# Kernel tuning notes

Measured on AMD Instinct MI355X. Metric: run time of the kernel, lower is better.

Reference implementation:

```python
import jax, jax.numpy as jnp
import numpy as np

N = 512
D = 400          # per-sample feature dim (lstm_hidden_dim * 2)
H = 400          # hidden dim of F_func (lstm_hidden_dim * 2)


def setup_inputs() -> dict:
    key = jax.random.key(0)
    k1, k2, k3, k4, k5, k6 = jax.random.split(key, 6)
    x_samples = jax.random.normal(k1, (N, D), dtype=jnp.float32)
    y_samples = jax.random.normal(k2, (N, D), dtype=jnp.float32)
    # torch nn.Linear default init: U(-1/sqrt(fan_in), 1/sqrt(fan_in))
    b1_bound = 1.0 / np.sqrt(2 * D)
    b2_bound = 1.0 / np.sqrt(H)
    W1 = jax.random.uniform(k3, (H, 2 * D), minval=-b1_bound, maxval=b1_bound, dtype=jnp.float32)
    b1 = jax.random.uniform(k4, (H,), minval=-b1_bound, maxval=b1_bound, dtype=jnp.float32)
    W2 = jax.random.uniform(k5, (1, H), minval=-b2_bound, maxval=b2_bound, dtype=jnp.float32)
    b2 = jax.random.uniform(k6, (1,), minval=-b2_bound, maxval=b2_bound, dtype=jnp.float32)
    return {"x_samples": x_samples, "y_samples": y_samples,
            "W1": W1, "b1": b1, "W2": W2, "b2": b2}


def reference(x_samples, y_samples, W1, b1, W2, b2):
    n = y_samples.shape[0]
    W1x, W1y = W1[:, :D], W1[:, D:]
    hx = x_samples @ W1x.T          # [N, H], contribution of x
    hy = y_samples @ W1y.T          # [N, H], contribution of y

    def score(h):  # second linear + softplus, squeeze out last dim of 1
        return jax.nn.softplus(h @ W2.T + b2)[..., 0]

    # T0[i] = F(x[i], y[i])
    T0 = score(jax.nn.relu(hx + hy + b1))                      # [N]
    # T1[i, j] = F(x[j], y[i])  (x tiled along dim 0, y along dim 1)
    h_pair = jax.nn.relu(hy[:, None, :] + hx[None, :, :] + b1) # [N, N, H]
    T1 = score(h_pair)                                          # [N, N]

    t0_mean = T0.mean()
    lower_bound = t0_mean - (jax.nn.logsumexp(T1, axis=1).mean() - jnp.log(jnp.float32(n)))
    upper_bound = t0_mean - T1.mean()
    return (lower_bound, upper_bound)
```

## Files before the change

kernel.cpp:

```cpp
#include <hip/hip_runtime.h>
#include <math.h>


#define NSAMP 512
#define DIM 400
#define HID 400

__global__ __launch_bounds__(256) void club_gemm_kernel(
    const float* __restrict__ X, const float* __restrict__ Y,
    const float* __restrict__ W1, const float* __restrict__ b1,
    float* __restrict__ hxT8, float* __restrict__ hyb)
{
    __shared__ __align__(16) float Ls[64 * 204];
    const int t    = threadIdx.x;
    const int lane = t & 63;
    const int wave = __builtin_amdgcn_readfirstlane(t >> 6);
    const int b    = blockIdx.x;

    const float* __restrict__ Lbase;
    const float* __restrict__ Sbase;
    int Lstride, Lcol0, Lrow0, Lrowmax, Sstride, srow_base;
    int kh, mat;

    if (b < 400) {
        mat = 0; kh = b & 1;
        const int bx = (b >> 1) & 7, by = b >> 4;
        Lbase = X;  Lstride = DIM;     Lcol0 = 0;   Lrow0 = bx * 64; Lrowmax = NSAMP - 1;
        Sbase = W1; Sstride = 2 * DIM;
        srow_base = by * 16 + wave * 4;
    } else {
        mat = 1;
        const int bb = b - 400; kh = bb & 1;
        const int bx = (bb >> 1) & 31, by = bb >> 6;
        Lbase = W1; Lstride = 2 * DIM; Lcol0 = DIM; Lrow0 = by * 64; Lrowmax = HID - 1;
        Sbase = Y;  Sstride = DIM;
        srow_base = bx * 16 + wave * 4;
    }
    const int kc0 = kh * 200;

    for (int idx = t; idx < 3200; idx += 256) {
        int row = idx / 50, q = idx % 50;
        int r = Lrow0 + row; if (r > Lrowmax) r = Lrowmax;
        float4 v = *(const float4*)(Lbase + (size_t)r * Lstride + Lcol0 + kc0 + 4 * q);
        *(float4*)(Ls + row * 204 + 4 * q) = v;
    }
    __syncthreads();

    float acc[4] = {0.f, 0.f, 0.f, 0.f};
#pragma unroll 2
    for (int k4 = 0; k4 < 50; k4++) {
        float4 xv = *(const float4*)(Ls + lane * 204 + 4 * k4);
#pragma unroll
        for (int c = 0; c < 4; c++) {
            const float* __restrict__ wp =
                Sbase + (size_t)(srow_base + c) * Sstride + Lcol0 - (mat ? DIM : 0)
                      + (mat ? 0 : 0) + kc0 + 4 * k4;
            float4 wv = *(const float4*)(Sbase + (size_t)(srow_base + c) * Sstride + kc0 + 4 * k4);
            (void)wp;
            acc[c] = fmaf(xv.x, wv.x, acc[c]);
            acc[c] = fmaf(xv.y, wv.y, acc[c]);
            acc[c] = fmaf(xv.z, wv.z, acc[c]);
            acc[c] = fmaf(xv.w, wv.w, acc[c]);
        }
    }

    if (mat == 0) {
        const int j = Lrow0 + lane;
        float* __restrict__ base =
            hxT8 + (size_t)(srow_base >> 3) * 4096 + (size_t)j * 8 + (srow_base & 4);
#pragma unroll
        for (int c = 0; c < 4; c++)
            atomicAdd(base + c, acc[c]);
    } else {
        const int h = Lrow0 + lane;
        if (h < HID) {
            if (kh == 0) {
                float bv = b1[h];
#pragma unroll
                for (int c = 0; c < 4; c++) acc[c] += bv;
            }
#pragma unroll
            for (int c = 0; c < 4; c++)
                atomicAdd(hyb + (size_t)(srow_base + c) * HID + h, acc[c]);
        }
    }
}

__global__ __launch_bounds__(256) void club_pair_kernel(
    const float* __restrict__ hxT8, const float* __restrict__ hyb,
    const float* __restrict__ W2, const float* __restrict__ b2,
    double* __restrict__ expsum, double* __restrict__ tsum,
    double* __restrict__ diagT)
{
    const int t    = threadIdx.x;
    const int lane = t & 63;
    const int wave = __builtin_amdgcn_readfirstlane(t >> 6);
    const int jx   = blockIdx.x;
    const int j    = jx * 64 + lane;
    const int i    = blockIdx.y * 4 + wave;

    const float* __restrict__ Bp = hxT8 + (size_t)j * 8;
    const float* __restrict__ Ap = hyb + (size_t)i * HID;

    float acc0 = 0.f, acc1 = 0.f;
#pragma unroll 2
    for (int g = 0; g < 50; g++) {
        const int h = 8 * g;
        float4 b0 = *(const float4*)(Bp + (size_t)g * 4096);
        float4 b1v = *(const float4*)(Bp + (size_t)g * 4096 + 4);
        float4 a0 = *(const float4*)(Ap + h);
        float4 a1 = *(const float4*)(Ap + h + 4);
        float4 w0 = *(const float4*)(W2 + h);
        float4 w1 = *(const float4*)(W2 + h + 4);
        acc0 = fmaf(fmaxf(a0.x + b0.x, 0.f), w0.x, acc0);
        acc1 = fmaf(fmaxf(a0.y + b0.y, 0.f), w0.y, acc1);
        acc0 = fmaf(fmaxf(a0.z + b0.z, 0.f), w0.z, acc0);
        acc1 = fmaf(fmaxf(a0.w + b0.w, 0.f), w0.w, acc1);
        acc0 = fmaf(fmaxf(a1.x + b1v.x, 0.f), w1.x, acc0);
        acc1 = fmaf(fmaxf(a1.y + b1v.y, 0.f), w1.y, acc1);
        acc0 = fmaf(fmaxf(a1.z + b1v.z, 0.f), w1.z, acc0);
        acc1 = fmaf(fmaxf(a1.w + b1v.w, 0.f), w1.w, acc1);
    }

    float s  = (acc0 + acc1) + b2[0];
    float es = expf(s);
    float T  = log1pf(es);
    if (j == i) diagT[i] = (double)T;
    double eD = 1.0 + (double)es;
    double tD = (double)T;
    for (int off = 32; off > 0; off >>= 1) {
        eD += __shfl_down(eD, off);
        tD += __shfl_down(tD, off);
    }
    if (lane == 0) {
        expsum[i * 8 + jx] = eD;
        tsum  [i * 8 + jx] = tD;
    }
}

__global__ __launch_bounds__(512) void club_final_kernel(
    const double* __restrict__ expsum, const double* __restrict__ tsum,
    const double* __restrict__ diagT, float* __restrict__ out)
{
    __shared__ double sh[3 * 512];
    const int t = threadIdx.x;
    double es = 0.0, ts = 0.0;
#pragma unroll
    for (int b = 0; b < 8; b++) { es += expsum[t * 8 + b]; ts += tsum[t * 8 + b]; }
    sh[t] = log(es); sh[512 + t] = ts; sh[1024 + t] = diagT[t];
    __syncthreads();
    for (int off = 256; off > 0; off >>= 1) {
        if (t < off) {
            sh[t]        += sh[t + off];
            sh[512 + t]  += sh[512 + t + off];
            sh[1024 + t] += sh[1024 + t + off];
        }
        __syncthreads();
    }
    if (t == 0) {
        double t0m  = sh[1024] / 512.0;
        double lsem = sh[0]    / 512.0;
        double t1m  = sh[512]  / (512.0 * 512.0);
        out[0] = (float)(t0m - (lsem - log(512.0)));
        out[1] = (float)(t0m - t1m);
    }
}

extern "C" void kernel_launch(void* const* d_in, const int* in_sizes, int n_in,
                              void* d_out, int out_size, void* d_ws, size_t ws_size,
                              hipStream_t stream) {
    const float* X  = (const float*)d_in[0];
    const float* Y  = (const float*)d_in[1];
    const float* W1 = (const float*)d_in[2];
    const float* b1 = (const float*)d_in[3];
    const float* W2 = (const float*)d_in[4];
    const float* b2 = (const float*)d_in[5];
    float* out = (float*)d_out;

    char* ws = (char*)d_ws;
    float*  hxT8   = (float*) (ws);
    float*  hyb    = (float*) (ws +  819200);
    double* expsum = (double*)(ws + 1638400);
    double* tsum   = (double*)(ws + 1671168);
    double* diagT  = (double*)(ws + 1703936);

    hipMemsetAsync(ws, 0, 1638400, stream);

    club_gemm_kernel <<<dim3(848),    256, 0, stream>>>(X, Y, W1, b1, hxT8, hyb);
    club_pair_kernel <<<dim3(8, 128), 256, 0, stream>>>(hxT8, hyb, W2, b2,
                                                        expsum, tsum, diagT);
    club_final_kernel<<<1, 512, 0, stream>>>(expsum, tsum, diagT, out);
}
```

Measured before the change: 112.2 us.

## Drop memset and atomics, fuse final reduction into pair kernel via last-block counter

The GEMM kernel now loops over both K halves itself and writes results directly instead of splitting K and accumulating with atomicAdd. This removes the workspace memset. The pair kernel computes four rows of i per wave group and splits H across two waves, combining the halves through shared memory so each hx load is reused across rows. The separate final kernel is replaced by a last-block-done counter that runs the reduction inside the pair kernel. Together these cut launches and atomics. In exchange the GEMM reads more operand data per block, and the counter reset depends on the GEMM kernel running first.

```diff
diff --git a/kernel.cpp b/kernel.cpp
--- a/kernel.cpp
+++ b/kernel.cpp
@@ -9,79 +9,76 @@
 __global__ __launch_bounds__(256) void club_gemm_kernel(
     const float* __restrict__ X, const float* __restrict__ Y,
     const float* __restrict__ W1, const float* __restrict__ b1,
-    float* __restrict__ hxT8, float* __restrict__ hyb)
+    float* __restrict__ hxT8, float* __restrict__ hyb,
+    unsigned int* __restrict__ counter)
 {
     __shared__ __align__(16) float Ls[64 * 204];
     const int t    = threadIdx.x;
     const int lane = t & 63;
     const int wave = __builtin_amdgcn_readfirstlane(t >> 6);
     const int b    = blockIdx.x;
+    if (b == 0 && t == 0) *counter = 0u;
 
     const float* __restrict__ Lbase;
     const float* __restrict__ Sbase;
-    int Lstride, Lcol0, Lrow0, Lrowmax, Sstride, srow_base;
-    int kh, mat;
+    int Lstride, Lcol0, Lrow0, Lrowmax, Sstride, sr0;
+    int mat;
 
     if (b < 400) {
-        mat = 0; kh = b & 1;
-        const int bx = (b >> 1) & 7, by = b >> 4;
+        mat = 0;
+        const int bx = b & 7, by = b >> 3;
         Lbase = X;  Lstride = DIM;     Lcol0 = 0;   Lrow0 = bx * 64; Lrowmax = NSAMP - 1;
         Sbase = W1; Sstride = 2 * DIM;
-        srow_base = by * 16 + wave * 4;
+        sr0 = by * 8 + wave * 2;
     } else {
         mat = 1;
-        const int bb = b - 400; kh = bb & 1;
-        const int bx = (bb >> 1) & 31, by = bb >> 6;
+        const int bb = b - 400;
+        const int bx = bb & 63, by = bb >> 6;
         Lbase = W1; Lstride = 2 * DIM; Lcol0 = DIM; Lrow0 = by * 64; Lrowmax = HID - 1;
         Sbase = Y;  Sstride = DIM;
-        srow_base = bx * 16 + wave * 4;
-    }
-    const int kc0 = kh * 200;
-
-    for (int idx = t; idx < 3200; idx += 256) {
-        int row = idx / 50, q = idx % 50;
-        int r = Lrow0 + row; if (r > Lrowmax) r = Lrowmax;
-        float4 v = *(const float4*)(Lbase + (size_t)r * Lstride + Lcol0 + kc0 + 4 * q);
-        *(float4*)(Ls + row * 204 + 4 * q) = v;
-    }
-    __syncthreads();
-
-    float acc[4] = {0.f, 0.f, 0.f, 0.f};
+        sr0 = bx * 8 + wave * 2;
+    }
+
+    float acc0 = 0.f, acc1 = 0.f;
+
+    for (int kc = 0; kc < DIM; kc += 200) {
+        __syncthreads();
+        for (int idx = t; idx < 3200; idx += 256) {
+            int row = idx / 50, q = idx % 50;
+            int r = Lrow0 + row; if (r > Lrowmax) r = Lrowmax;
+            float4 v = *(const float4*)(Lbase + (size_t)r * Lstride + Lcol0 + kc + 4 * q);
+            *(float4*)(Ls + row * 204 + 4 * q) = v;
+        }
+        __syncthreads();
+        const float* __restrict__ w0p = Sbase + (size_t)sr0 * Sstride + kc;
+        const float* __restrict__ w1p = Sbase + (size_t)(sr0 + 1) * Sstride + kc;
 #pragma unroll 2
-    for (int k4 = 0; k4 < 50; k4++) {
-        float4 xv = *(const float4*)(Ls + lane * 204 + 4 * k4);
-#pragma unroll
-        for (int c = 0; c < 4; c++) {
-            const float* __restrict__ wp =
-                Sbase + (size_t)(srow_base + c) * Sstride + Lcol0 - (mat ? DIM : 0)
-                      + (mat ? 0 : 0) + kc0 + 4 * k4;
-            float4 wv = *(const float4*)(Sbase + (size_t)(srow_base + c) * Sstride + kc0 + 4 * k4);
-            (void)wp;
-            acc[c] = fmaf(xv.x, wv.x, acc[c]);
-            acc[c] = fmaf(xv.y, wv.y, acc[c]);
-            acc[c] = fmaf(xv.z, wv.z, acc[c]);
-            acc[c] = fmaf(xv.w, wv.w, acc[c]);
+        for (int k4 = 0; k4 < 50; k4++) {
+            float4 xv = *(const float4*)(Ls + lane * 204 + 4 * k4);
+            float4 wa = *(const float4*)(w0p + 4 * k4);
+            float4 wb = *(const float4*)(w1p + 4 * k4);
+            acc0 = fmaf(xv.x, wa.x, acc0);
+            acc0 = fmaf(xv.y, wa.y, acc0);
+            acc0 = fmaf(xv.z, wa.z, acc0);
+            acc0 = fmaf(xv.w, wa.w, acc0);
+            acc1 = fmaf(xv.x, wb.x, acc1);
+            acc1 = fmaf(xv.y, wb.y, acc1);
+            acc1 = fmaf(xv.z, wb.z, acc1);
+            acc1 = fmaf(xv.w, wb.w, acc1);
         }
     }
 
     if (mat == 0) {
+        const int g = sr0 >> 3;
         const int j = Lrow0 + lane;
-        float* __restrict__ base =
-            hxT8 + (size_t)(srow_base >> 3) * 4096 + (size_t)j * 8 + (srow_base & 4);
-#pragma unroll
-        for (int c = 0; c < 4; c++)
-            atomicAdd(base + c, acc[c]);
+        *(float2*)(hxT8 + ((size_t)g * NSAMP + j) * 8 + (sr0 & 7)) =
+            make_float2(acc0, acc1);
     } else {
         const int h = Lrow0 + lane;
         if (h < HID) {
-            if (kh == 0) {
-                float bv = b1[h];
-#pragma unroll
-                for (int c = 0; c < 4; c++) acc[c] += bv;
-            }
-#pragma unroll
-            for (int c = 0; c < 4; c++)
-                atomicAdd(hyb + (size_t)(srow_base + c) * HID + h, acc[c]);
+            float bv = b1[h];
+            hyb[(size_t)sr0 * HID + h]       = acc0 + bv;
+            hyb[(size_t)(sr0 + 1) * HID + h] = acc1 + bv;
         }
     }
 }
@@ -90,77 +87,106 @@
     const float* __restrict__ hxT8, const float* __restrict__ hyb,
     const float* __restrict__ W2, const float* __restrict__ b2,
     double* __restrict__ expsum, double* __restrict__ tsum,
-    double* __restrict__ diagT)
+    double* __restrict__ diagT, unsigned int* __restrict__ counter,
+    float* __restrict__ out)
 {
+    __shared__ float C[4][4][64];
+    __shared__ double R[3 * 256];
+    __shared__ bool isLast;
+
     const int t    = threadIdx.x;
     const int lane = t & 63;
     const int wave = __builtin_amdgcn_readfirstlane(t >> 6);
+    const int grp  = wave >> 1, half = wave & 1;
     const int jx   = blockIdx.x;
     const int j    = jx * 64 + lane;
-    const int i    = blockIdx.y * 4 + wave;
-
-    const float* __restrict__ Bp = hxT8 + (size_t)j * 8;
-    const float* __restrict__ Ap = hyb + (size_t)i * HID;
-
-    float acc0 = 0.f, acc1 = 0.f;
-#pragma unroll 2
-    for (int g = 0; g < 50; g++) {
-        const int h = 8 * g;
-        float4 b0 = *(const float4*)(Bp + (size_t)g * 4096);
-        float4 b1v = *(const float4*)(Bp + (size_t)g * 4096 + 4);
-        float4 a0 = *(const float4*)(Ap + h);
-        float4 a1 = *(const float4*)(Ap + h + 4);
-        float4 w0 = *(const float4*)(W2 + h);
-        float4 w1 = *(const float4*)(W2 + h + 4);
-        acc0 = fmaf(fmaxf(a0.x + b0.x, 0.f), w0.x, acc0);
-        acc1 = fmaf(fmaxf(a0.y + b0.y, 0.f), w0.y, acc1);
-        acc0 = fmaf(fmaxf(a0.z + b0.z, 0.f), w0.z, acc0);
-        acc1 = fmaf(fmaxf(a0.w + b0.w, 0.f), w0.w, acc1);
-        acc0 = fmaf(fmaxf(a1.x + b1v.x, 0.f), w1.x, acc0);
-        acc1 = fmaf(fmaxf(a1.y + b1v.y, 0.f), w1.y, acc1);
-        acc0 = fmaf(fmaxf(a1.z + b1v.z, 0.f), w1.z, acc0);
-        acc1 = fmaf(fmaxf(a1.w + b1v.w, 0.f), w1.w, acc1);
-    }
-
-    float s  = (acc0 + acc1) + b2[0];
-    float es = expf(s);
-    float T  = log1pf(es);
-    if (j == i) diagT[i] = (double)T;
-    double eD = 1.0 + (double)es;
-    double tD = (double)T;
-    for (int off = 32; off > 0; off >>= 1) {
-        eD += __shfl_down(eD, off);
-        tD += __shfl_down(tD, off);
-    }
-    if (lane == 0) {
-        expsum[i * 8 + jx] = eD;
-        tsum  [i * 8 + jx] = tD;
-    }
-}
-
-__global__ __launch_bounds__(512) void club_final_kernel(
-    const double* __restrict__ expsum, const double* __restrict__ tsum,
-    const double* __restrict__ diagT, float* __restrict__ out)
-{
-    __shared__ double sh[3 * 512];
-    const int t = threadIdx.x;
-    double es = 0.0, ts = 0.0;
-#pragma unroll
-    for (int b = 0; b < 8; b++) { es += expsum[t * 8 + b]; ts += tsum[t * 8 + b]; }
-    sh[t] = log(es); sh[512 + t] = ts; sh[1024 + t] = diagT[t];
-    __syncthreads();
-    for (int off = 256; off > 0; off >>= 1) {
+    const int i0   = blockIdx.y * 8 + grp * 4;
+
+    const float* __restrict__ Ap = hyb + (size_t)i0 * HID + half * 200;
+    const float* __restrict__ Bp = hxT8 + (size_t)(half * 25) * 4096 + (size_t)j * 8;
+    const float* __restrict__ Wp = W2 + half * 200;
+
+    float acc[4] = {0.f, 0.f, 0.f, 0.f};
+
+#pragma unroll 5
+    for (int g = 0; g < 25; g++) {
+        const float* __restrict__ bb = Bp + (size_t)g * 4096;
+        float4 b0 = *(const float4*)(bb);
+        float4 b1v = *(const float4*)(bb + 4);
+        float4 w0 = *(const float4*)(Wp + 8 * g);
+        float4 w1 = *(const float4*)(Wp + 8 * g + 4);
+#pragma unroll
+        for (int c = 0; c < 4; c++) {
+            const float* __restrict__ ap = Ap + (size_t)c * HID + 8 * g;
+            float4 a0 = *(const float4*)(ap);
+            float4 a1 = *(const float4*)(ap + 4);
+            acc[c] = fmaf(fmaxf(a0.x + b0.x, 0.f), w0.x, acc[c]);
+            acc[c] = fmaf(fmaxf(a0.y + b0.y, 0.f), w0.y, acc[c]);
+            acc[c] = fmaf(fmaxf(a0.z + b0.z, 0.f), w0.z, acc[c]);
+            acc[c] = fmaf(fmaxf(a0.w + b0.w, 0.f), w0.w, acc[c]);
+            acc[c] = fmaf(fmaxf(a1.x + b1v.x, 0.f), w1.x, acc[c]);
+            acc[c] = fmaf(fmaxf(a1.y + b1v.y, 0.f), w1.y, acc[c]);
+            acc[c] = fmaf(fmaxf(a1.z + b1v.z, 0.f), w1.z, acc[c]);
+            acc[c] = fmaf(fmaxf(a1.w + b1v.w, 0.f), w1.w, acc[c]);
+        }
+    }
+
+#pragma unroll
+    for (int c = 0; c < 4; c++) C[wave][c][lane] = acc[c];
+    __syncthreads();
+
+    if (half == 0) {
+        const float bb2 = b2[0];
+#pragma unroll
+        for (int c = 0; c < 4; c++) {
+            const int i = i0 + c;
+            float s  = C[wave][c][lane] + C[wave + 1][c][lane] + bb2;
+            float es = expf(s);
+            float T  = log1pf(es);
+            if (j == i) diagT[i] = (double)T;
+            double eD = 1.0 + (double)es;
+            double tD = (double)T;
+            for (int off = 32; off > 0; off >>= 1) {
+                eD += __shfl_down(eD, off);
+                tD += __shfl_down(tD, off);
+            }
+            if (lane == 0) {
+                expsum[i * 8 + jx] = eD;
+                tsum  [i * 8 + jx] = tD;
+            }
+        }
+    }
+
+    __threadfence();
+    __syncthreads();
+    if (t == 0) isLast = (atomicAdd(counter, 1u) == 511u);
+    __syncthreads();
+    if (!isLast) return;
+    __threadfence();
+
+    double lse = 0.0, tsm = 0.0, dg = 0.0;
+    for (int i = t; i < NSAMP; i += 256) {
+        double es = 0.0, ts = 0.0;
+#pragma unroll
+        for (int bq = 0; bq < 8; bq++) { es += expsum[i * 8 + bq]; ts += tsum[i * 8 + bq]; }
+        lse += log(es);
+        tsm += ts;
+        dg  += diagT[i];
+    }
+    R[t] = lse; R[256 + t] = tsm; R[512 + t] = dg;
+    __syncthreads();
+    for (int off = 128; off > 0; off >>= 1) {
         if (t < off) {
-            sh[t]        += sh[t + off];
-            sh[512 + t]  += sh[512 + t + off];
-            sh[1024 + t] += sh[1024 + t + off];
+            R[t]       += R[t + off];
+            R[256 + t] += R[256 + t + off];
+            R[512 + t] += R[512 + t + off];
         }
         __syncthreads();
     }
     if (t == 0) {
-        double t0m  = sh[1024] / 512.0;
-        double lsem = sh[0]    / 512.0;
-        double t1m  = sh[512]  / (512.0 * 512.0);
+        double t0m  = R[512] / 512.0;
+        double lsem = R[0]   / 512.0;
+        double t1m  = R[256] / (512.0 * 512.0);
         out[0] = (float)(t0m - (lsem - log(512.0)));
         out[1] = (float)(t0m - t1m);
     }
@@ -178,16 +204,14 @@
     float* out = (float*)d_out;
 
     char* ws = (char*)d_ws;
-    float*  hxT8   = (float*) (ws);
-    float*  hyb    = (float*) (ws +  819200);
-    double* expsum = (double*)(ws + 1638400);
-    double* tsum   = (double*)(ws + 1671168);
-    double* diagT  = (double*)(ws + 1703936);
-
-    hipMemsetAsync(ws, 0, 1638400, stream);
-
-    club_gemm_kernel <<<dim3(848),    256, 0, stream>>>(X, Y, W1, b1, hxT8, hyb);
-    club_pair_kernel <<<dim3(8, 128), 256, 0, stream>>>(hxT8, hyb, W2, b2,
-                                                        expsum, tsum, diagT);
-    club_final_kernel<<<1, 512, 0, stream>>>(expsum, tsum, diagT, out);
+    float*        hxT8    = (float*) (ws);
+    float*        hyb     = (float*) (ws +  819200);
+    double*       expsum  = (double*)(ws + 1638400);
+    double*       tsum    = (double*)(ws + 1671168);
+    double*       diagT   = (double*)(ws + 1703936);
+    unsigned int* counter = (unsigned int*)(ws + 1708032);
+
+    club_gemm_kernel<<<dim3(848),   256, 0, stream>>>(X, Y, W1, b1, hxT8, hyb, counter);
+    club_pair_kernel<<<dim3(8, 64), 256, 0, stream>>>(hxT8, hyb, W2, b2,
+                                                      expsum, tsum, diagT, counter, out);
 }
```

Result: slower. 150.0 us (+33.6%).
